# Kernel optimization log

Hardware: AMD Instinct MI355X
Metric: run time of the kernel (lower is better)

## Reference

```python
import jax, jax.numpy as jnp
import numpy as np

B, T, C, H = 8, 2048, 1024, 64  # batch, time(block_size), n_embd, head_size


def setup_inputs() -> dict:
    key = jax.random.key(0)
    k1, k2, k3, k4 = jax.random.split(key, 4)
    x = jax.random.normal(k1, (B, T, C), dtype=jnp.float32)
    # nn.Linear(n_embd, head_size, bias=False): y = x @ W.T with W [H, C];
    # store as [C, H] so projection is x @ W.
    Wq = jax.random.normal(k2, (C, H), dtype=jnp.float32) * 0.02
    Wk = jax.random.normal(k3, (C, H), dtype=jnp.float32) * 0.02
    Wv = jax.random.normal(k4, (C, H), dtype=jnp.float32) * 0.02
    return {"x": x, "Wq": Wq, "Wk": Wk, "Wv": Wv}


def reference(x, Wq, Wk, Wv):
    # x: [B, T, C]
    Bb, Tt, Cc = x.shape
    q = x @ Wq  # [B, T, H]
    k = x @ Wk  # [B, T, H]
    v = x @ Wv  # [B, T, H]
    # scores = Q @ K^T / sqrt(channels)  -- note: code scales by n_embd, not head_size
    scale = jnp.asarray(Cc, x.dtype) ** 0.5
    scores = jnp.einsum('bth,bsh->bts', q, k) / scale  # [B, T, T]
    # causal mask (decoder=True): lower-triangular allowed
    causal = jnp.tril(jnp.ones((Tt, Tt), dtype=bool))
    scores = jnp.where(causal, scores, -jnp.inf)
    attn = jax.nn.softmax(scores, axis=-1)  # [B, T, T]
    # dropout p=0.0 -> identity
    res = attn @ v  # [B, T, H]
    return res, attn
```

## Files before the change

### kernel.cpp

```cpp
#include <hip/hip_runtime.h>
#include <hip/hip_bf16.h>


typedef __attribute__((ext_vector_type(8))) short bf16x8;
typedef __attribute__((ext_vector_type(4))) float f32x4;

#define NB 8
#define NT 2048
#define NC 1024
#define NH 64

__device__ __forceinline__ unsigned short f2bf(float f) {
    unsigned int u = __builtin_bit_cast(unsigned int, f);
    u += 0x7fffu + ((u >> 16) & 1u);
    return (unsigned short)(u >> 16);
}

__device__ __forceinline__ bf16x8 cvt8(float4 a, float4 b) {
    union { bf16x8 v; __hip_bfloat162 h[4]; } u;
    u.h[0] = __float22bfloat162_rn(make_float2(a.x, a.y));
    u.h[1] = __float22bfloat162_rn(make_float2(a.z, a.w));
    u.h[2] = __float22bfloat162_rn(make_float2(b.x, b.y));
    u.h[3] = __float22bfloat162_rn(make_float2(b.z, b.w));
    return u.v;
}

__device__ __forceinline__ void async_ld16(const void* g, const void* l) {
    __builtin_amdgcn_global_load_lds(
        (const __attribute__((address_space(1))) unsigned int*)g,
        (__attribute__((address_space(3))) unsigned int*)(unsigned int)(unsigned long long)l,
        16, 0, 0);
}

__global__ __launch_bounds__(256) void wt_kernel(
        const float* __restrict__ Wq,
        const float* __restrict__ Wk,
        const float* __restrict__ Wv,
        unsigned short* __restrict__ Wt) {
    __shared__ float tile[64][65];
    int m  = blockIdx.x >> 4;
    int k0 = (blockIdx.x & 15) * 64;
    const float* W = (m == 0) ? Wq : ((m == 1) ? Wk : Wv);
    int tid = threadIdx.x;
    for (int i = 0; i < 4; ++i) {
        int f = tid + i * 256;
        int r = f >> 4, c4 = (f & 15) * 4;
        float4 v = *(const float4*)&W[(size_t)(k0 + r) * 64 + c4];
        tile[r][c4 + 0] = v.x; tile[r][c4 + 1] = v.y;
        tile[r][c4 + 2] = v.z; tile[r][c4 + 3] = v.w;
    }
    __syncthreads();
    int n  = tid & 63;
    int kq = (tid >> 6) * 16;
    float scale = (m == 0) ? 0.03125f : 1.0f;
    __attribute__((aligned(16))) unsigned short outv[16];
    for (int j = 0; j < 16; ++j)
        outv[j] = f2bf(tile[kq + j][n] * scale);
    unsigned short* dst = &Wt[(size_t)m * (64 * 1024) + (size_t)n * 1024 + k0 + kq];
    *(uint4*)dst       = *(const uint4*)&outv[0];
    *(uint4*)(dst + 8) = *(const uint4*)&outv[8];
}

__global__ __launch_bounds__(256) void qkv_kernel(
        const float* __restrict__ x,
        const unsigned short* __restrict__ Wt,
        unsigned short* __restrict__ qkv,
        unsigned short* __restrict__ v_t) {
    __shared__ float At[32 * 64];
    __shared__ unsigned short Bt[192 * 64];
    char* Ab = (char*)At;
    char* Bb = (char*)Bt;

    int tid  = threadIdx.x;
    int wave = tid >> 6, lane = tid & 63, quad = lane >> 4, l15 = lane & 15;
    int row0 = blockIdx.x * 32;

    f32x4 acc[2][3];
#pragma unroll
    for (int rt = 0; rt < 2; ++rt)
#pragma unroll
        for (int j = 0; j < 3; ++j) acc[rt][j] = (f32x4){0.f, 0.f, 0.f, 0.f};

    for (int kb = 0; kb < 16; ++kb) {
        __syncthreads();
#pragma unroll
        for (int i = 0; i < 2; ++i) {
            int s = i * 256 + tid;
            int m = s >> 4, p = s & 15;
            int j = (p & 8) | ((p & 7) ^ (m & 7));
            async_ld16(x + (size_t)(row0 + m) * NC + kb * 64 + j * 4,
                       Ab + i * 4096 + wave * 1024);
        }
#pragma unroll
        for (int i = 0; i < 6; ++i) {
            int s = i * 256 + tid;
            int n = s >> 3, p = s & 7;
            int j = p ^ (n & 7);
            async_ld16(Wt + (size_t)n * NC + kb * 64 + j * 8,
                       Bb + i * 4096 + wave * 1024);
        }
        __syncthreads();

#pragma unroll
        for (int c = 0; c < 2; ++c) {
            bf16x8 af[2];
#pragma unroll
            for (int rt = 0; rt < 2; ++rt) {
                int m  = rt * 16 + l15;
                int j0 = c * 8 + quad * 2;
                int p0 = (j0 & 8) | ((j0 & 7) ^ (m & 7));
                int p1 = (j0 & 8) | (((j0 + 1) & 7) ^ (m & 7));
                float4 a0 = *(const float4*)(Ab + m * 256 + p0 * 16);
                float4 a1 = *(const float4*)(Ab + m * 256 + p1 * 16);
                af[rt] = cvt8(a0, a1);
            }
#pragma unroll
            for (int jj = 0; jj < 3; ++jj) {
                int n = (wave * 3 + jj) * 16 + l15;
                int p = (c * 4 + quad) ^ (n & 7);
                bf16x8 bf = *(const bf16x8*)(Bb + n * 128 + p * 16);
#pragma unroll
                for (int rt = 0; rt < 2; ++rt)
                    acc[rt][jj] = __builtin_amdgcn_mfma_f32_16x16x32_bf16(
                        af[rt], bf, acc[rt][jj], 0, 0, 0);
            }
        }
    }

    int b = row0 >> 11;
#pragma unroll
    for (int jj = 0; jj < 3; ++jj) {
        int g   = wave * 3 + jj;
        int mat = g >> 2;
        int col = (g & 3) * 16 + l15;
#pragma unroll
        for (int rt = 0; rt < 2; ++rt) {
            int rowb = row0 + rt * 16 + quad * 4;
            if (mat < 2) {
#pragma unroll
                for (int r = 0; r < 4; ++r)
                    qkv[(size_t)mat * (16384 * 64) + (size_t)(rowb + r) * 64 + col] =
                        f2bf(acc[rt][jj][r]);
            } else {
                union { unsigned long long q; unsigned short us[4]; } pk;
#pragma unroll
                for (int r = 0; r < 4; ++r) pk.us[r] = f2bf(acc[rt][jj][r]);
                *(unsigned long long*)&v_t[((size_t)b * 64 + col) * NT + (rowb & 2047)] = pk.q;
            }
        }
    }
}

__global__ __launch_bounds__(256) void attn_u_kernel(
        const unsigned short* __restrict__ qg,
        const unsigned short* __restrict__ kg,
        const unsigned short* __restrict__ vtg,
        float* __restrict__ l,
        float* __restrict__ res,
        float* __restrict__ attn) {
    __shared__ unsigned short kt[64 * 64];
    __shared__ unsigned short vt[64 * 64];
    __shared__ float ptf[4 * 16 * 68];
    char* ktb = (char*)kt;
    char* vtb = (char*)vt;

    int tid  = threadIdx.x;
    int wave = tid >> 6, lane = tid & 63, quad = lane >> 4, l15 = lane & 15;
    int it = blockIdx.x >> 2, qq = blockIdx.x & 3;
    int b  = blockIdx.y;
    if (qq > it) return;
    int t0 = it * 64;
    size_t brow = (size_t)b * NT;

    bf16x8 qf[2];
    {
        const unsigned short* qp = qg + (brow + t0 + wave * 16 + l15) * NH + quad * 8;
        qf[0] = *(const bf16x8*)qp;
        qf[1] = *(const bf16x8*)(qp + 32);
    }
    int trow[4];
#pragma unroll
    for (int r = 0; r < 4; ++r) trow[r] = t0 + wave * 16 + quad * 4 + r;

    f32x4 oacc[4];
#pragma unroll
    for (int nt = 0; nt < 4; ++nt) oacc[nt] = (f32x4){0.f, 0.f, 0.f, 0.f};
    float rs[4] = {0.f, 0.f, 0.f, 0.f};

    for (int st = qq; st <= it; st += 4) {
        __syncthreads();
#pragma unroll
        for (int i = 0; i < 2; ++i) {
            int s = i * 256 + tid;
            int r = s >> 3, p = s & 7;
            int j = p ^ (r & 7);
            async_ld16(kg + (brow + st * 64 + r) * NH + j * 8,
                       ktb + i * 4096 + wave * 1024);
        }
#pragma unroll
        for (int i = 0; i < 2; ++i) {
            int s = i * 256 + tid;
            int r = s >> 3, p = s & 7;
            int j = p ^ (r & 7);
            async_ld16(vtg + ((size_t)b * 64 + r) * NT + st * 64 + j * 8,
                       vtb + i * 4096 + wave * 1024);
        }
        __syncthreads();

        f32x4 sacc[4];
#pragma unroll
        for (int nt = 0; nt < 4; ++nt) sacc[nt] = (f32x4){0.f, 0.f, 0.f, 0.f};
#pragma unroll
        for (int c = 0; c < 2; ++c)
#pragma unroll
            for (int nt = 0; nt < 4; ++nt) {
                int n = nt * 16 + l15;
                int p = (c * 4 + quad) ^ (n & 7);
                bf16x8 kf = *(const bf16x8*)(ktb + n * 128 + p * 16);
                sacc[nt] = __builtin_amdgcn_mfma_f32_16x16x32_bf16(qf[c], kf, sacc[nt], 0, 0, 0);
            }

        bool dia = (st == it);
#pragma unroll
        for (int nt = 0; nt < 4; ++nt) {
            int s_g = st * 64 + nt * 16 + l15;
#pragma unroll
            for (int r = 0; r < 4; ++r) {
                float e = __expf(sacc[nt][r]);
                if (dia && s_g > trow[r]) e = 0.f;
                rs[r] += e;
                ptf[wave * 1088 + (quad * 4 + r) * 68 + nt * 16 + l15] = e;
            }
        }
        asm volatile("s_waitcnt lgkmcnt(0)" ::: "memory");

#pragma unroll
        for (int r = 0; r < 4; ++r) {
            int row = quad * 4 + r;
            float4 pv = *(const float4*)&ptf[wave * 1088 + row * 68 + l15 * 4];
            *(float4*)&attn[(brow + t0 + wave * 16 + row) * NT + st * 64 + l15 * 4] = pv;
        }

#pragma unroll
        for (int c = 0; c < 2; ++c) {
            const float* pp = &ptf[wave * 1088 + l15 * 68 + c * 32 + quad * 8];
            float4 a0 = *(const float4*)pp;
            float4 a1 = *(const float4*)(pp + 4);
            bf16x8 pf = cvt8(a0, a1);
#pragma unroll
            for (int nt = 0; nt < 4; ++nt) {
                int n = nt * 16 + l15;
                int p = (c * 4 + quad) ^ (n & 7);
                bf16x8 vf = *(const bf16x8*)(vtb + n * 128 + p * 16);
                oacc[nt] = __builtin_amdgcn_mfma_f32_16x16x32_bf16(pf, vf, oacc[nt], 0, 0, 0);
            }
        }
    }

#pragma unroll
    for (int r = 0; r < 4; ++r) {
        float v = rs[r];
        v += __shfl_xor(v, 1, 16);
        v += __shfl_xor(v, 2, 16);
        v += __shfl_xor(v, 4, 16);
        v += __shfl_xor(v, 8, 16);
        if (l15 == 0)
            unsafeAtomicAdd(&l[brow + trow[r]], v);
    }

#pragma unroll
    for (int nt = 0; nt < 4; ++nt)
#pragma unroll
        for (int r = 0; r < 4; ++r)
            unsafeAtomicAdd(&res[(brow + trow[r]) * NH + nt * 16 + l15], oacc[nt][r]);
}

__global__ __launch_bounds__(256) void finalize_kernel(
        const float* __restrict__ l,
        float* __restrict__ res,
        float* __restrict__ attn) {
    __shared__ float rinv[64];
    int bx = blockIdx.x;
    int it = bx >> 5, st = bx & 31;
    int b  = blockIdx.y;
    size_t brow = (size_t)b * NT;
    int t0 = it * 64;
    int tid = threadIdx.x;

    if (st > it) {
        float4 z4 = {0.f, 0.f, 0.f, 0.f};
#pragma unroll
        for (int k = 0; k < 4; ++k) {
            int f = tid + k * 256;
            int r = f >> 4, c4 = (f & 15) * 4;
            *(float4*)&attn[(brow + t0 + r) * NT + st * 64 + c4] = z4;
        }
        return;
    }

    if (tid < 64) rinv[tid] = 1.0f / l[brow + t0 + tid];
    __syncthreads();

#pragma unroll
    for (int k = 0; k < 4; ++k) {
        int f = tid + k * 256;
        int r = f >> 4, c4 = (f & 15) * 4;
        float* p = &attn[(brow + t0 + r) * NT + st * 64 + c4];
        float4 v = *(const float4*)p;
        float s = rinv[r];
        v.x *= s; v.y *= s; v.z *= s; v.w *= s;
        *(float4*)p = v;
    }

    if (st == it) {
#pragma unroll
        for (int k = 0; k < 4; ++k) {
            int f = tid + k * 256;
            int r = f >> 4, c4 = (f & 15) * 4;
            float* p = &res[(brow + t0 + r) * NH + c4];
            float4 v = *(const float4*)p;
            float s = rinv[r];
            v.x *= s; v.y *= s; v.z *= s; v.w *= s;
            *(float4*)p = v;
        }
    }
}

extern "C" void kernel_launch(void* const* d_in, const int* in_sizes, int n_in,
                              void* d_out, int out_size, void* d_ws, size_t ws_size,
                              hipStream_t stream) {
    const float* x  = (const float*)d_in[0];
    const float* Wq = (const float*)d_in[1];
    const float* Wk = (const float*)d_in[2];
    const float* Wv = (const float*)d_in[3];

    unsigned short* ws  = (unsigned short*)d_ws;
    unsigned short* Wt  = ws;
    unsigned short* qkv = ws + 3 * 64 * 1024;
    unsigned short* v_t = qkv + 2 * 16384 * 64;
    float* l = (float*)(v_t + 16384 * 64);

    float* res  = (float*)d_out;
    float* attn = res + (size_t)NB * NT * NH;

    hipMemsetAsync(l, 0, (size_t)NB * NT * sizeof(float), stream);
    hipMemsetAsync(res, 0, (size_t)NB * NT * NH * sizeof(float), stream);

    hipLaunchKernelGGL(wt_kernel, dim3(48), dim3(256), 0, stream, Wq, Wk, Wv, Wt);
    hipLaunchKernelGGL(qkv_kernel, dim3(512), dim3(256), 0, stream, x, Wt, qkv, v_t);

    const unsigned short* qg = qkv;
    const unsigned short* kg = qkv + 16384 * 64;

    hipLaunchKernelGGL(attn_u_kernel, dim3(128, 8), dim3(256), 0, stream,
                       qg, kg, v_t, l, res, attn);
    hipLaunchKernelGGL(finalize_kernel, dim3(1024, 8), dim3(256), 0, stream,
                       l, res, attn);
}
```

Before: 236.3 us.

## Load MFMA B operands straight from global and double-buffer x tiles

In the QKV projection, the x tile is now double-buffered in shared memory, so the next tile's async load overlaps the current MFMAs. The weight fragments are read directly from global memory into registers instead of being staged through LDS. In the attention kernel, the K and V^T fragments are likewise loaded straight from global memory per wave, which removes the shared-memory staging and two block barriers per iteration. This trades LDS traffic and barrier stalls for redundant global/L2 reads across waves, more register pressure, and exposed global load latency.

Result: slower. 281.8 us (+19.2%).

```diff
diff --git a/kernel.cpp b/kernel.cpp
--- a/kernel.cpp
+++ b/kernel.cpp
@@ -66,10 +66,8 @@
         const unsigned short* __restrict__ Wt,
         unsigned short* __restrict__ qkv,
         unsigned short* __restrict__ v_t) {
-    __shared__ float At[32 * 64];
-    __shared__ unsigned short Bt[192 * 64];
+    __shared__ float At[2 * 32 * 64];
     char* Ab = (char*)At;
-    char* Bb = (char*)Bt;
 
     int tid  = threadIdx.x;
     int wave = tid >> 6, lane = tid & 63, quad = lane >> 4, l15 = lane & 15;
@@ -81,26 +79,36 @@
 #pragma unroll
         for (int j = 0; j < 3; ++j) acc[rt][j] = (f32x4){0.f, 0.f, 0.f, 0.f};
 
+#pragma unroll
+    for (int i = 0; i < 2; ++i) {
+        int s = i * 256 + tid;
+        int m = s >> 4, p = s & 15;
+        int j = (p & 8) | ((p & 7) ^ (m & 7));
+        async_ld16(x + (size_t)(row0 + m) * NC + j * 4,
+                   Ab + i * 4096 + wave * 1024);
+    }
+    __syncthreads();
+
+    int cur = 0;
     for (int kb = 0; kb < 16; ++kb) {
-        __syncthreads();
-#pragma unroll
-        for (int i = 0; i < 2; ++i) {
-            int s = i * 256 + tid;
-            int m = s >> 4, p = s & 15;
-            int j = (p & 8) | ((p & 7) ^ (m & 7));
-            async_ld16(x + (size_t)(row0 + m) * NC + kb * 64 + j * 4,
-                       Ab + i * 4096 + wave * 1024);
-        }
-#pragma unroll
-        for (int i = 0; i < 6; ++i) {
-            int s = i * 256 + tid;
-            int n = s >> 3, p = s & 7;
-            int j = p ^ (n & 7);
-            async_ld16(Wt + (size_t)n * NC + kb * 64 + j * 8,
-                       Bb + i * 4096 + wave * 1024);
-        }
-        __syncthreads();
-
+        if (kb < 15) {
+#pragma unroll
+            for (int i = 0; i < 2; ++i) {
+                int s = i * 256 + tid;
+                int m = s >> 4, p = s & 15;
+                int j = (p & 8) | ((p & 7) ^ (m & 7));
+                async_ld16(x + (size_t)(row0 + m) * NC + (kb + 1) * 64 + j * 4,
+                           Ab + (cur ^ 1) * 8192 + i * 4096 + wave * 1024);
+            }
+        }
+        bf16x8 bfr[2][3];
+#pragma unroll
+        for (int jj = 0; jj < 3; ++jj) {
+            int n = (wave * 3 + jj) * 16 + l15;
+            const unsigned short* bp = Wt + (size_t)n * NC + kb * 64 + quad * 8;
+            bfr[0][jj] = *(const bf16x8*)bp;
+            bfr[1][jj] = *(const bf16x8*)(bp + 32);
+        }
 #pragma unroll
         for (int c = 0; c < 2; ++c) {
             bf16x8 af[2];
@@ -110,21 +118,19 @@
                 int j0 = c * 8 + quad * 2;
                 int p0 = (j0 & 8) | ((j0 & 7) ^ (m & 7));
                 int p1 = (j0 & 8) | (((j0 + 1) & 7) ^ (m & 7));
-                float4 a0 = *(const float4*)(Ab + m * 256 + p0 * 16);
-                float4 a1 = *(const float4*)(Ab + m * 256 + p1 * 16);
+                float4 a0 = *(const float4*)(Ab + cur * 8192 + m * 256 + p0 * 16);
+                float4 a1 = *(const float4*)(Ab + cur * 8192 + m * 256 + p1 * 16);
                 af[rt] = cvt8(a0, a1);
             }
 #pragma unroll
-            for (int jj = 0; jj < 3; ++jj) {
-                int n = (wave * 3 + jj) * 16 + l15;
-                int p = (c * 4 + quad) ^ (n & 7);
-                bf16x8 bf = *(const bf16x8*)(Bb + n * 128 + p * 16);
+            for (int jj = 0; jj < 3; ++jj)
 #pragma unroll
                 for (int rt = 0; rt < 2; ++rt)
                     acc[rt][jj] = __builtin_amdgcn_mfma_f32_16x16x32_bf16(
-                        af[rt], bf, acc[rt][jj], 0, 0, 0);
-            }
-        }
+                        af[rt], bfr[c][jj], acc[rt][jj], 0, 0, 0);
+        }
+        __syncthreads();
+        cur ^= 1;
     }
 
     int b = row0 >> 11;
@@ -158,11 +164,7 @@
         float* __restrict__ l,
         float* __restrict__ res,
         float* __restrict__ attn) {
-    __shared__ unsigned short kt[64 * 64];
-    __shared__ unsigned short vt[64 * 64];
     __shared__ float ptf[4 * 16 * 68];
-    char* ktb = (char*)kt;
-    char* vtb = (char*)vt;
 
     int tid  = threadIdx.x;
     int wave = tid >> 6, lane = tid & 63, quad = lane >> 4, l15 = lane & 15;
@@ -188,24 +190,14 @@
     float rs[4] = {0.f, 0.f, 0.f, 0.f};
 
     for (int st = qq; st <= it; st += 4) {
-        __syncthreads();
-#pragma unroll
-        for (int i = 0; i < 2; ++i) {
-            int s = i * 256 + tid;
-            int r = s >> 3, p = s & 7;
-            int j = p ^ (r & 7);
-            async_ld16(kg + (brow + st * 64 + r) * NH + j * 8,
-                       ktb + i * 4096 + wave * 1024);
-        }
-#pragma unroll
-        for (int i = 0; i < 2; ++i) {
-            int s = i * 256 + tid;
-            int r = s >> 3, p = s & 7;
-            int j = p ^ (r & 7);
-            async_ld16(vtg + ((size_t)b * 64 + r) * NT + st * 64 + j * 8,
-                       vtb + i * 4096 + wave * 1024);
-        }
-        __syncthreads();
+        bf16x8 kf[2][4];
+#pragma unroll
+        for (int nt = 0; nt < 4; ++nt) {
+            const unsigned short* kp =
+                kg + (brow + st * 64 + nt * 16 + l15) * NH + quad * 8;
+            kf[0][nt] = *(const bf16x8*)kp;
+            kf[1][nt] = *(const bf16x8*)(kp + 32);
+        }
 
         f32x4 sacc[4];
 #pragma unroll
@@ -213,12 +205,18 @@
 #pragma unroll
         for (int c = 0; c < 2; ++c)
 #pragma unroll
-            for (int nt = 0; nt < 4; ++nt) {
-                int n = nt * 16 + l15;
-                int p = (c * 4 + quad) ^ (n & 7);
-                bf16x8 kf = *(const bf16x8*)(ktb + n * 128 + p * 16);
-                sacc[nt] = __builtin_amdgcn_mfma_f32_16x16x32_bf16(qf[c], kf, sacc[nt], 0, 0, 0);
-            }
+            for (int nt = 0; nt < 4; ++nt)
+                sacc[nt] = __builtin_amdgcn_mfma_f32_16x16x32_bf16(
+                    qf[c], kf[c][nt], sacc[nt], 0, 0, 0);
+
+        bf16x8 vf[2][4];
+#pragma unroll
+        for (int nt = 0; nt < 4; ++nt) {
+            const unsigned short* vp =
+                vtg + ((size_t)b * 64 + nt * 16 + l15) * NT + st * 64 + quad * 8;
+            vf[0][nt] = *(const bf16x8*)vp;
+            vf[1][nt] = *(const bf16x8*)(vp + 32);
+        }
 
         bool dia = (st == it);
 #pragma unroll
@@ -248,12 +246,9 @@
             float4 a1 = *(const float4*)(pp + 4);
             bf16x8 pf = cvt8(a0, a1);
 #pragma unroll
-            for (int nt = 0; nt < 4; ++nt) {
-                int n = nt * 16 + l15;
-                int p = (c * 4 + quad) ^ (n & 7);
-                bf16x8 vf = *(const bf16x8*)(vtb + n * 128 + p * 16);
-                oacc[nt] = __builtin_amdgcn_mfma_f32_16x16x32_bf16(pf, vf, oacc[nt], 0, 0, 0);
-            }
+            for (int nt = 0; nt < 4; ++nt)
+                oacc[nt] = __builtin_amdgcn_mfma_f32_16x16x32_bf16(
+                    pf, vf[c][nt], oacc[nt], 0, 0, 0);
         }
     }
 
```
